# Kernel tuning notes

Measured on AMD Instinct MI355X. Metric: run time of the kernel, lower is better.

Reference implementation:

```python
import jax, jax.numpy as jnp
import numpy as np

L, B, H, Y, C = 256, 256, 256, 32, 16  # seq len, batch, hidden, y_size, spline channels (u_size+1)


def setup_inputs() -> dict:
    key = jax.random.key(0)
    ks = jax.random.split(key, 10)
    # times: uniform grid 0..L-1 (torchcde default spline parameterization), shape (L,B,1)
    ts = jnp.broadcast_to(jnp.arange(L, dtype=jnp.float32)[:, None, None], (L, B, 1))
    us = jax.random.normal(ks[0], (L, B, C - 1), dtype=jnp.float32)
    h0 = 0.1 * jax.random.normal(ks[1], (B, H), dtype=jnp.float32)
    s = 1.0 / np.sqrt(H)
    # NCDEFunc: Linear(H,H) -> relu -> Linear(H, H*C) -> tanh -> view(B,H,C)
    W1 = jax.random.uniform(ks[2], (H, H), jnp.float32, -s, s)
    b1 = jax.random.uniform(ks[3], (H,), jnp.float32, -s, s)
    W2 = jax.random.uniform(ks[4], (H, H * C), jnp.float32, -s, s)
    b2 = jax.random.uniform(ks[5], (H * C,), jnp.float32, -s, s)
    # decoder MLP(H, 2H, Y, 1): Linear(H,2H) -> tanh -> Linear(2H,Y)
    dW1 = jax.random.uniform(ks[6], (H, 2 * H), jnp.float32, -s, s)
    db1 = jax.random.uniform(ks[7], (2 * H,), jnp.float32, -s, s)
    s2 = 1.0 / np.sqrt(2 * H)
    dW2 = jax.random.uniform(ks[8], (2 * H, Y), jnp.float32, -s2, s2)
    db2 = jax.random.uniform(ks[9], (Y,), jnp.float32, -s2, s2)
    return dict(ts=ts, us=us, h0=h0, W1=W1, b1=b1, W2=W2, b2=b2,
                dW1=dW1, db1=db1, dW2=dW2, db2=db2)


def reference(ts, us, h0, W1, b1, W2, b2, dW1, db1, dW2, db2):
    # permute to batch-first and build control path x: (B, L, C)
    xb = jnp.concatenate([jnp.transpose(ts, (1, 0, 2)), jnp.transpose(us, (1, 0, 2))], axis=2)
    # hermite cubic with backward differences on unit grid (torchcde default t=arange):
    # node derivative d_i = x_i - x_{i-1} (delta=1); d_0 = d_1
    diffs = xb[:, 1:] - xb[:, :-1]                      # (B, L-1, C)
    dnode = jnp.concatenate([diffs[:, :1], diffs], axis=1)  # (B, L, C)
    t = ts[:, 0, 0]  # (L,) -- cdeint t grid = ts.squeeze(-1)[0,:] after permute

    def dXdt(s_):
        # derivative of the hermite cubic spline at scalar time s_ (unit knot spacing)
        idx = jnp.clip(jnp.floor(s_).astype(jnp.int32), 0, L - 2)
        tau = s_ - idx.astype(s_.dtype)
        xi, xip = xb[:, idx], xb[:, idx + 1]            # (B, C)
        di, dip = dnode[:, idx], dnode[:, idx + 1]
        h00p = 6.0 * tau * tau - 6.0 * tau              # h01' = -h00'
        h10p = 3.0 * tau * tau - 4.0 * tau + 1.0
        h11p = 3.0 * tau * tau - 2.0 * tau
        return h00p * (xi - xip) + h10p * di + h11p * dip  # (B, C)

    def vf(z):
        # NCDEFunc: z (B,H) -> matrix (B,H,C)
        hid = jax.nn.relu(z @ W1 + b1)
        return jnp.tanh(hid @ W2 + b2).reshape(B, H, C)

    def step(z, inp):
        s_, dt_ = inp
        dz = jnp.einsum('bhc,bc->bh', vf(z), dXdt(s_))  # f(z) @ dX/dt
        zn = z + dt_ * dz                               # Euler update on grid t
        return zn, zn

    _, zs = jax.lax.scan(step, h0, (t[:-1], t[1:] - t[:-1]))
    z_seq = jnp.concatenate([h0[None], zs], axis=0)     # (L, B, H): cdeint output at all t
    # decoder then permute(1,0,2) -> already time-major here: (L, B, Y)
    return jnp.tanh(z_seq @ dW1 + db1) @ dW2 + db2
```

## Files before the change

### kernel.cpp

```cpp
#include <hip/hip_runtime.h>
#include <math.h>

#define LL 256
#define BB 256
#define HH 256
#define CC 16
#define YY 32
#define HC (HH*CC)
#define NSTEP (LL-1)
#define NBG 32
#define BGB 8
#define HCH 32
#define TPB 1024
#define NJS 8

__device__ __forceinline__ float fast_tanh(float x) {
    float e = __expf(2.0f * x);
    return 1.0f - 2.0f / (e + 1.0f);
}

__device__ __forceinline__ float ld_coh(const float* p) {
    return __hip_atomic_load(p, __ATOMIC_RELAXED, __HIP_MEMORY_SCOPE_AGENT);
}
__device__ __forceinline__ float2 ld_coh2(const float* p) {
    union { unsigned long long u; float2 f; } cv;
    cv.u = __hip_atomic_load((const unsigned long long*)p,
                             __ATOMIC_RELAXED, __HIP_MEMORY_SCOPE_AGENT);
    return cv.f;
}
__device__ __forceinline__ void st_coh(float* p, float v) {
    __hip_atomic_store(p, v, __ATOMIC_RELAXED, __HIP_MEMORY_SCOPE_AGENT);
}

__device__ __forceinline__ void bg_barrier(unsigned* cnt, unsigned target) {
    __syncthreads();
    if (threadIdx.x == 0) {
        __hip_atomic_fetch_add(cnt, 1u, __ATOMIC_RELAXED, __HIP_MEMORY_SCOPE_AGENT);
        while (__hip_atomic_load(cnt, __ATOMIC_RELAXED, __HIP_MEMORY_SCOPE_AGENT) < target)
            __builtin_amdgcn_s_sleep(2);
    }
    __syncthreads();
}

__global__ void __launch_bounds__(TPB)
k_scan(const float* __restrict__ us, const float* __restrict__ W1,
       const float* __restrict__ b1, const float* __restrict__ W2,
       const float* __restrict__ b2, float* __restrict__ zs,
       float* __restrict__ hidG, unsigned* __restrict__ barG) {
    __shared__ float smem[NJS * BGB * 512 + 2048 + 2048 + 512 + 128 + 32];
    float* psum  = smem;
    float* pa    = smem;
    float* z_loc = smem + NJS * BGB * 512;
    float* hidT  = z_loc + BGB * HH;
    float* b2s   = hidT + HH * BGB;
    float* dvs   = b2s + 512;
    float* b1s   = dvs + 128;

    const int bg = blockIdx.x >> 3;
    const int hc = blockIdx.x & 7;
    const int t  = threadIdx.x;
    const int b0 = bg * BGB;
    const int h0 = hc * HCH;
    const int n0 = h0 * CC;

    const int ajc = t >> 5;
    const int ah  = t & 31;
    float w1r[8];
    #pragma unroll
    for (int r = 0; r < 8; r++)
        w1r[r] = W1[(size_t)(ajc * 8 + r) * HH + h0 + ah];
    for (int i = t; i < 512; i += TPB) b2s[i] = b2[n0 + i];
    if (t < HCH) b1s[t] = b1[h0 + t];
    __syncthreads();

    unsigned* cnt = barG + (size_t)bg * 64;

    const int sb  = t >> 7;
    const int sj2 = (t & 127) << 1;
    const int jsp = t >> 7;
    const int ct  = (t & 127) << 2;
    const int col = t & 511;
    const int bh  = (t >> 9) << 2;

    for (int k = 0; k < NSTEP; k++) {
        const size_t zk = (size_t)k * (BB * HH);

        {
            float2 v = ld_coh2(&zs[zk + (size_t)(b0 + sb) * HH + sj2]);
            *(float2*)&z_loc[sb * HH + sj2] = v;
        }
        if (t < BGB * CC) {
            int b = t >> 4, c = t & 15;
            int kk = (k < 1) ? 1 : k;
            float v = 1.0f;
            if (c > 0)
                v = us[((size_t)kk * BB + b0 + b) * (CC - 1) + c - 1]
                  - us[((size_t)(kk - 1) * BB + b0 + b) * (CC - 1) + c - 1];
            dvs[b * CC + c] = v;
        }
        __syncthreads();

        {
            float acc[BGB];
            #pragma unroll
            for (int b = 0; b < BGB; b++) acc[b] = 0.f;
            #pragma unroll
            for (int r2 = 0; r2 < 2; r2++) {
                #pragma unroll
                for (int b = 0; b < BGB; b++) {
                    float4 zv = *(const float4*)&z_loc[b * HH + ajc * 8 + r2 * 4];
                    acc[b] += zv.x * w1r[r2 * 4 + 0] + zv.y * w1r[r2 * 4 + 1]
                            + zv.z * w1r[r2 * 4 + 2] + zv.w * w1r[r2 * 4 + 3];
                }
            }
            #pragma unroll
            for (int b = 0; b < BGB; b++)
                pa[ajc * 256 + b * HCH + ah] = acc[b];
        }
        __syncthreads();
        if (t < BGB * HCH) {
            float s = b1s[t & 31];
            #pragma unroll
            for (int q = 0; q < 32; q++) s += pa[q * 256 + t];
            st_coh(&hidG[(size_t)(b0 + (t >> 5)) * HH + h0 + (t & 31)],
                   fmaxf(s, 0.f));
        }
        bg_barrier(cnt, 8u * (2u * (unsigned)k + 1u));

        {
            float2 v = ld_coh2(&hidG[(size_t)(b0 + sb) * HH + sj2]);
            hidT[sj2 * BGB + sb]       = v.x;
            hidT[(sj2 + 1) * BGB + sb] = v.y;
        }
        __syncthreads();

        {
            float4 acc[BGB];
            #pragma unroll
            for (int b = 0; b < BGB; b++) acc[b] = make_float4(0.f, 0.f, 0.f, 0.f);
            const int jb = jsp * 32;
            const float* w2p = &W2[(size_t)jb * HC + n0 + ct];
            #pragma unroll 4
            for (int j = 0; j < 32; j++) {
                float4 hA = *(const float4*)&hidT[(jb + j) * BGB];
                float4 hB = *(const float4*)&hidT[(jb + j) * BGB + 4];
                float4 w  = *(const float4*)&w2p[(size_t)j * HC];
                acc[0].x += hA.x * w.x; acc[0].y += hA.x * w.y;
                acc[0].z += hA.x * w.z; acc[0].w += hA.x * w.w;
                acc[1].x += hA.y * w.x; acc[1].y += hA.y * w.y;
                acc[1].z += hA.y * w.z; acc[1].w += hA.y * w.w;
                acc[2].x += hA.z * w.x; acc[2].y += hA.z * w.y;
                acc[2].z += hA.z * w.z; acc[2].w += hA.z * w.w;
                acc[3].x += hA.w * w.x; acc[3].y += hA.w * w.y;
                acc[3].z += hA.w * w.z; acc[3].w += hA.w * w.w;
                acc[4].x += hB.x * w.x; acc[4].y += hB.x * w.y;
                acc[4].z += hB.x * w.z; acc[4].w += hB.x * w.w;
                acc[5].x += hB.y * w.x; acc[5].y += hB.y * w.y;
                acc[5].z += hB.y * w.z; acc[5].w += hB.y * w.w;
                acc[6].x += hB.z * w.x; acc[6].y += hB.z * w.y;
                acc[6].z += hB.z * w.z; acc[6].w += hB.z * w.w;
                acc[7].x += hB.w * w.x; acc[7].y += hB.w * w.y;
                acc[7].z += hB.w * w.z; acc[7].w += hB.w * w.w;
            }
            #pragma unroll
            for (int b = 0; b < BGB; b++)
                *(float4*)&psum[((jsp * BGB + b) << 9) + ct] = acc[b];
        }
        __syncthreads();

        {
            #pragma unroll
            for (int q = 0; q < 4; q++) {
                int b = bh + q;
                float g = b2s[col];
                #pragma unroll
                for (int s = 0; s < NJS; s++)
                    g += psum[((s * BGB + b) << 9) + col];
                float v = fast_tanh(g) * dvs[b * CC + (col & 15)];
                v += __shfl_xor(v, 1);
                v += __shfl_xor(v, 2);
                v += __shfl_xor(v, 4);
                v += __shfl_xor(v, 8);
                if ((col & 15) == 0) {
                    int hl = col >> 4;
                    st_coh(&zs[zk + (size_t)(BB * HH) + (size_t)(b0 + b) * HH + h0 + hl],
                           z_loc[b * HH + h0 + hl] + v);
                }
            }
        }
        bg_barrier(cnt, 8u * (2u * (unsigned)k + 2u));
    }
}

__global__ void k_out(const float* __restrict__ zseq, const float* __restrict__ dW1,
                      const float* __restrict__ db1, const float* __restrict__ dW2,
                      const float* __restrict__ db2, float* __restrict__ out) {
    __shared__ float zt[16][HH];
    __shared__ float act[16][2 * HH];
    int r0 = blockIdx.x * 16;
    int t  = threadIdx.x;
    {
        const float4* src = (const float4*)(zseq + (size_t)r0 * HH);
        float4* dst = (float4*)&zt[0][0];
        for (int i = t; i < 1024; i += 256) dst[i] = src[i];
    }
    __syncthreads();
    {
        int c0  = (t & 127) * 4;
        int rr0 = (t >> 7) * 8;
        float a[8][4];
        #pragma unroll
        for (int i = 0; i < 8; i++)
            #pragma unroll
            for (int q = 0; q < 4; q++) a[i][q] = 0.f;
        for (int j = 0; j < HH; j++) {
            float4 w = *(const float4*)&dW1[(size_t)j * 2 * HH + c0];
            #pragma unroll
            for (int i = 0; i < 8; i++) {
                float zv = zt[rr0 + i][j];
                a[i][0] += zv * w.x; a[i][1] += zv * w.y;
                a[i][2] += zv * w.z; a[i][3] += zv * w.w;
            }
        }
        float4 bias = *(const float4*)&db1[c0];
        #pragma unroll
        for (int i = 0; i < 8; i++) {
            act[rr0 + i][c0 + 0] = fast_tanh(a[i][0] + bias.x);
            act[rr0 + i][c0 + 1] = fast_tanh(a[i][1] + bias.y);
            act[rr0 + i][c0 + 2] = fast_tanh(a[i][2] + bias.z);
            act[rr0 + i][c0 + 3] = fast_tanh(a[i][3] + bias.w);
        }
    }
    __syncthreads();
    {
        int rl = t >> 4;
        int y2 = t & 15;
        float o0 = 0.f, o1 = 0.f;
        #pragma unroll 4
        for (int j = 0; j < 2 * HH; j++) {
            float av = act[rl][j];
            float2 w = *(const float2*)&dW2[(size_t)j * YY + y2 * 2];
            o0 += av * w.x; o1 += av * w.y;
        }
        float2 bias = *(const float2*)&db2[y2 * 2];
        out[(size_t)(r0 + rl) * YY + y2 * 2]     = o0 + bias.x;
        out[(size_t)(r0 + rl) * YY + y2 * 2 + 1] = o1 + bias.y;
    }
}

extern "C" void kernel_launch(void* const* d_in, const int* in_sizes, int n_in,
                              void* d_out, int out_size, void* d_ws, size_t ws_size,
                              hipStream_t stream) {
    const float* us  = (const float*)d_in[1];
    const float* h0  = (const float*)d_in[2];
    const float* W1  = (const float*)d_in[3];
    const float* b1  = (const float*)d_in[4];
    const float* W2  = (const float*)d_in[5];
    const float* b2  = (const float*)d_in[6];
    const float* dW1 = (const float*)d_in[7];
    const float* db1 = (const float*)d_in[8];
    const float* dW2 = (const float*)d_in[9];
    const float* db2 = (const float*)d_in[10];
    float* out = (float*)d_out;

    float* zs   = (float*)d_ws;
    float* hidG = zs + (size_t)LL * BB * HH;
    unsigned* barG = (unsigned*)(hidG + (size_t)BB * HH);

    hipMemcpyAsync(zs, h0, (size_t)BB * HH * sizeof(float),
                   hipMemcpyDeviceToDevice, stream);
    hipMemsetAsync(barG, 0, NBG * 64 * sizeof(unsigned), stream);

    k_scan<<<NBG * 8, TPB, 0, stream>>>(us, W1, b1, W2, b2, zs, hidG, barG);
    k_out<<<LL * BB / 16, 256, 0, stream>>>(zs, dW1, db1, dW2, db2, out);
}
```

Measured before the change: 3.624 ms.

## Compute full hidden layer redundantly per block to drop one grid barrier per step

Each of the 8 blocks in a batch group now computes the full 256-wide first layer (z@W1+b1, relu) itself instead of a 32-column slice that was exchanged through a global buffer. This removes the global hidG write/read and one of the two inter-block barriers per time step. In exchange each block does 8x the W1 work and streams all of W1 from global/L2 every step instead of keeping a slice in registers.

```diff
diff --git a/kernel.cpp b/kernel.cpp
--- a/kernel.cpp
+++ b/kernel.cpp
@@ -13,15 +13,13 @@
 #define HCH 32
 #define TPB 1024
 #define NJS 8
+#define AJS 16
 
 __device__ __forceinline__ float fast_tanh(float x) {
     float e = __expf(2.0f * x);
     return 1.0f - 2.0f / (e + 1.0f);
 }
 
-__device__ __forceinline__ float ld_coh(const float* p) {
-    return __hip_atomic_load(p, __ATOMIC_RELAXED, __HIP_MEMORY_SCOPE_AGENT);
-}
 __device__ __forceinline__ float2 ld_coh2(const float* p) {
     union { unsigned long long u; float2 f; } cv;
     cv.u = __hip_atomic_load((const unsigned long long*)p,
@@ -46,8 +44,8 @@
 k_scan(const float* __restrict__ us, const float* __restrict__ W1,
        const float* __restrict__ b1, const float* __restrict__ W2,
        const float* __restrict__ b2, float* __restrict__ zs,
-       float* __restrict__ hidG, unsigned* __restrict__ barG) {
-    __shared__ float smem[NJS * BGB * 512 + 2048 + 2048 + 512 + 128 + 32];
+       unsigned* __restrict__ barG) {
+    __shared__ float smem[NJS * BGB * 512 + 2048 + 2048 + 512 + 128 + 256];
     float* psum  = smem;
     float* pa    = smem;
     float* z_loc = smem + NJS * BGB * 512;
@@ -60,23 +58,18 @@
     const int hc = blockIdx.x & 7;
     const int t  = threadIdx.x;
     const int b0 = bg * BGB;
-    const int h0 = hc * HCH;
-    const int n0 = h0 * CC;
-
-    const int ajc = t >> 5;
-    const int ah  = t & 31;
-    float w1r[8];
-    #pragma unroll
-    for (int r = 0; r < 8; r++)
-        w1r[r] = W1[(size_t)(ajc * 8 + r) * HH + h0 + ah];
+    const int n0 = hc * HCH * CC;
+
     for (int i = t; i < 512; i += TPB) b2s[i] = b2[n0 + i];
-    if (t < HCH) b1s[t] = b1[h0 + t];
+    for (int i = t; i < HH; i += TPB) b1s[i] = b1[i];
     __syncthreads();
 
     unsigned* cnt = barG + (size_t)bg * 64;
 
     const int sb  = t >> 7;
     const int sj2 = (t & 127) << 1;
+    const int hq  = t & 63;
+    const int ajs = t >> 6;
     const int jsp = t >> 7;
     const int ct  = (t & 127) << 2;
     const int col = t & 511;
@@ -101,36 +94,34 @@
         __syncthreads();
 
         {
-            float acc[BGB];
-            #pragma unroll
-            for (int b = 0; b < BGB; b++) acc[b] = 0.f;
-            #pragma unroll
-            for (int r2 = 0; r2 < 2; r2++) {
+            float4 accA[BGB];
+            #pragma unroll
+            for (int b = 0; b < BGB; b++) accA[b] = make_float4(0.f, 0.f, 0.f, 0.f);
+            const float* w1p = &W1[(size_t)(ajs * 16) * HH + hq * 4];
+            #pragma unroll 4
+            for (int j = 0; j < 16; j++) {
+                float4 w = *(const float4*)&w1p[(size_t)j * HH];
                 #pragma unroll
                 for (int b = 0; b < BGB; b++) {
-                    float4 zv = *(const float4*)&z_loc[b * HH + ajc * 8 + r2 * 4];
-                    acc[b] += zv.x * w1r[r2 * 4 + 0] + zv.y * w1r[r2 * 4 + 1]
-                            + zv.z * w1r[r2 * 4 + 2] + zv.w * w1r[r2 * 4 + 3];
+                    float zv = z_loc[b * HH + ajs * 16 + j];
+                    accA[b].x += zv * w.x; accA[b].y += zv * w.y;
+                    accA[b].z += zv * w.z; accA[b].w += zv * w.w;
                 }
             }
             #pragma unroll
             for (int b = 0; b < BGB; b++)
-                pa[ajc * 256 + b * HCH + ah] = acc[b];
-        }
-        __syncthreads();
-        if (t < BGB * HCH) {
-            float s = b1s[t & 31];
-            #pragma unroll
-            for (int q = 0; q < 32; q++) s += pa[q * 256 + t];
-            st_coh(&hidG[(size_t)(b0 + (t >> 5)) * HH + h0 + (t & 31)],
-                   fmaxf(s, 0.f));
-        }
-        bg_barrier(cnt, 8u * (2u * (unsigned)k + 1u));
-
-        {
-            float2 v = ld_coh2(&hidG[(size_t)(b0 + sb) * HH + sj2]);
-            hidT[sj2 * BGB + sb]       = v.x;
-            hidT[(sj2 + 1) * BGB + sb] = v.y;
+                *(float4*)&pa[ajs * 2048 + b * 256 + hq * 4] = accA[b];
+        }
+        __syncthreads();
+        {
+            #pragma unroll
+            for (int rep = 0; rep < 2; rep++) {
+                int o = t + rep * 1024;
+                float s = b1s[o & 255];
+                #pragma unroll
+                for (int q = 0; q < AJS; q++) s += pa[q * 2048 + o];
+                hidT[(o & 255) * BGB + (o >> 8)] = fmaxf(s, 0.f);
+            }
         }
         __syncthreads();
 
@@ -183,12 +174,13 @@
                 v += __shfl_xor(v, 8);
                 if ((col & 15) == 0) {
                     int hl = col >> 4;
-                    st_coh(&zs[zk + (size_t)(BB * HH) + (size_t)(b0 + b) * HH + h0 + hl],
-                           z_loc[b * HH + h0 + hl] + v);
+                    int h = hc * HCH + hl;
+                    st_coh(&zs[zk + (size_t)(BB * HH) + (size_t)(b0 + b) * HH + h],
+                           z_loc[b * HH + h] + v);
                 }
             }
         }
-        bg_barrier(cnt, 8u * (2u * (unsigned)k + 2u));
+        bg_barrier(cnt, 8u * (unsigned)(k + 1));
     }
 }
 
@@ -264,13 +256,12 @@
     float* out = (float*)d_out;
 
     float* zs   = (float*)d_ws;
-    float* hidG = zs + (size_t)LL * BB * HH;
-    unsigned* barG = (unsigned*)(hidG + (size_t)BB * HH);
+    unsigned* barG = (unsigned*)(zs + (size_t)LL * BB * HH);
 
     hipMemcpyAsync(zs, h0, (size_t)BB * HH * sizeof(float),
                    hipMemcpyDeviceToDevice, stream);
     hipMemsetAsync(barG, 0, NBG * 64 * sizeof(unsigned), stream);
 
-    k_scan<<<NBG * 8, TPB, 0, stream>>>(us, W1, b1, W2, b2, zs, hidG, barG);
+    k_scan<<<NBG * 8, TPB, 0, stream>>>(us, W1, b1, W2, b2, zs, barG);
     k_out<<<LL * BB / 16, 256, 0, stream>>>(zs, dW1, db1, dW2, db2, out);
 }
```

Measured after the change: 4.231 ms. 16.8% more time.
